# Optimization experiments

Hardware: AMD Instinct MI355X
Metric: run time of the kernel (lower is better)

## Reference

```python
import jax, jax.numpy as jnp
import numpy as np

NUM_CLASSES = 10
HIDDEN = 64
_LABEL2MASK_THRESHOL = 500


def setup_inputs() -> dict:
    key = jax.random.key(0)
    ks = jax.random.split(key, 8)
    B, h, w = 4, 60, 80
    feature1 = jax.random.normal(ks[0], (B, 512, h, w), dtype=jnp.float32)
    feature2 = jax.random.normal(ks[1], (B, 512, h // 2, w // 2), dtype=jnp.float32)
    # kaiming fan_in init for 1x1 convs: std = sqrt(2/fan_in)
    w1 = jax.random.normal(ks[2], (HIDDEN, 512), dtype=jnp.float32) * np.sqrt(2.0 / 512)
    b1 = jnp.zeros((HIDDEN,), dtype=jnp.float32)
    w2 = jax.random.normal(ks[3], (HIDDEN, 512), dtype=jnp.float32) * np.sqrt(2.0 / 512)
    b2 = jnp.zeros((HIDDEN,), dtype=jnp.float32)
    wo = jax.random.normal(ks[4], (NUM_CLASSES + 1, HIDDEN), dtype=jnp.float32) * np.sqrt(2.0 / HIDDEN)
    bo = jnp.zeros((NUM_CLASSES + 1,), dtype=jnp.float32)
    return {"feature1": feature1, "feature2": feature2, "w1": w1, "b1": b1,
            "w2": w2, "b2": b2, "wo": wo, "bo": bo}


def conv1x1(x, w, b):
    # x: (B,C,H,W), w: (O,C) -> (B,O,H,W)
    return jnp.einsum('bchw,oc->bohw', x, w) + b[None, :, None, None]


def label2bbx(seg, num_classes):
    # seg: (B,H,W) int labels. Vectorized per-(batch,class) min/max reduction
    # replacing the original python double loop. Fixed output shape
    # (B*(num_classes-1), 6); rows failing the pixel-count threshold are -1.
    B, H, W = seg.shape
    classes = jnp.arange(1, num_classes)  # cls_id != 0, covers 1..num_classes-1
    mask = seg[:, None, :, :] == classes[None, :, None, None]  # (B,C-1,H,W)
    count = mask.sum(axis=(2, 3))
    xs = jnp.arange(W)
    ys = jnp.arange(H)
    big = jnp.int32(2 ** 30)
    xmin = jnp.where(mask, xs[None, None, None, :], big).min(axis=(2, 3))
    xmax = jnp.where(mask, xs[None, None, None, :], -1).max(axis=(2, 3))
    ymin = jnp.where(mask, ys[None, None, :, None], big).min(axis=(2, 3))
    ymax = jnp.where(mask, ys[None, None, :, None], -1).max(axis=(2, 3))
    valid = count >= _LABEL2MASK_THRESHOL
    batch_ids = jnp.broadcast_to(jnp.arange(B)[:, None], (B, num_classes - 1))
    cls_ids = jnp.broadcast_to(classes[None, :], (B, num_classes - 1))
    rows = jnp.stack([batch_ids, xmin, ymin, xmax, ymax, cls_ids], axis=-1)
    rows = jnp.where(valid[..., None], rows, -1)
    return rows.reshape(-1, 6)


def reference(feature1, feature2, w1, b1, w2, b2, wo, bo):
    feat1 = jax.nn.relu(conv1x1(feature1, w1, b1))          # (B,64,h,w)
    feat2 = jax.nn.relu(conv1x1(feature2, w2, b2))          # (B,64,h/2,w/2)
    feat2_up = jnp.repeat(jnp.repeat(feat2, 2, axis=2), 2, axis=3)
    combo = feat1 + feat2_up
    # nearest upsample scale_factor=8
    combo_up = jnp.repeat(jnp.repeat(combo, 8, axis=2), 8, axis=3)  # (B,64,8h,8w)
    out = jax.nn.relu(conv1x1(combo_up, wo, bo))            # (B,11,8h,8w)
    probability = jax.nn.softmax(out, axis=1)
    segmentation = jnp.argmax(probability, axis=1)
    bbx = label2bbx(segmentation, NUM_CLASSES)
    return probability, segmentation, bbx
```

## Files before the change

### kernel.cpp

```cpp
#include <hip/hip_runtime.h>
#include <math.h>

#define NB   4
#define CIN  512
#define HID  64
#define NK   11
#define HH1  60
#define W1p  80
#define P1   4800
#define HH2  30
#define W2p  40
#define P2   1200
#define HO   480
#define WOp  640
#define NP1  (NB*P1)
#define NP2  (NB*P2)
#define PLANE ((size_t)HO*WOp)
#define SEG_OFF ((size_t)NB*NK*PLANE)
#define BBX_OFF (SEG_OFF + (size_t)NB*PLANE)

#define WS_C1  65536
#define WS_F2  (WS_C1 + NP1*64)
#define WS_PRB (WS_F2 + NP2*64)
#define WS_SEG (WS_PRB + NP1*12)

typedef __attribute__((ext_vector_type(8))) short bf16x8;
typedef __attribute__((ext_vector_type(4))) float f32x4;

__device__ __forceinline__ unsigned short bfsplit(float x, float& resid) {
    unsigned u = __float_as_uint(x);
    unsigned t = u + 0x7FFFu + ((u >> 16) & 1u);
    unsigned short h = (unsigned short)(t >> 16);
    resid = x - __uint_as_float((unsigned)h << 16);
    return h;
}

__device__ __forceinline__ void gld16(const void* g, void* l) {
    __builtin_amdgcn_global_load_lds(
        (const __attribute__((address_space(1))) void*)g,
        (__attribute__((address_space(3))) void*)l, 16, 0, 0);
}

__global__ __launch_bounds__(256) void pack_w(const float* __restrict__ w1,
                                              const float* __restrict__ w2,
                                              float* __restrict__ ws) {
    int i = blockIdx.x * 256 + threadIdx.x;
    if (i >= HID * CIN) return;
    int o = i >> 9, c = i & 511;
    int chunk = c >> 6, r = c & 63, ks2 = r >> 5, k = r & 31;
    int lane = (o & 15) + ((k >> 3) << 4);
    int mt = o >> 4;
    int d = ((((chunk * 2 + ks2) * 4 + mt) * 2) * 64 + lane) * 8 + (k & 7);
    unsigned short* q = (unsigned short*)ws;
    float r1;
    unsigned short h = bfsplit(w1[i], r1);
    unsigned short m = bfsplit(r1, r1);
    q[d] = h; q[d + 512] = m;
    h = bfsplit(w2[i], r1); m = bfsplit(r1, r1);
    q[65536 + d] = h; q[65536 + d + 512] = m;
}

__global__ __launch_bounds__(256) void conv_mfma(const float* __restrict__ f1,
                                                 const float* __restrict__ f2,
                                                 const float* __restrict__ b1v,
                                                 const float* __restrict__ b2v,
                                                 const float* __restrict__ wsbase,
                                                 float* __restrict__ c1o,
                                                 float* __restrict__ f2o) {
    __shared__ float xraw[2][4096];
    __shared__ int   alds[2][4096];
    __shared__ int   xpl[4096];
    int t = blockIdx.x;
    const float* X; const float* bias; float* Cout; const int* WPK;
    int P, px0;
    const unsigned short* q = (const unsigned short*)wsbase;
    if (t < 300) {
        int b = t / 75, ti = t % 75;
        px0 = ti * 64;
        X = f1 + (size_t)b * CIN * P1;  P = P1;  bias = b1v;
        WPK = (const int*)q;
        Cout = c1o + (size_t)b * P1 * 64;
    } else {
        int u = t - 300; int b = u / 19, ti = u % 19;
        px0 = ti * 64; if (px0 > P2 - 64) px0 = P2 - 64;
        X = f2 + (size_t)b * CIN * P2;  P = P2;  bias = b2v;
        WPK = (const int*)(q + 65536);
        Cout = f2o + (size_t)b * P2 * 64;
    }
    int tid  = threadIdx.x;
    int lane = tid & 63;
    int wv   = tid >> 6;
    int pcol = lane & 15, kgrp = lane >> 4;

    auto dmaX = [&](int cc, int buf) {
#pragma unroll
        for (int qq = 0; qq < 4; ++qq) {
            int k = wv * 4 + qq;
            const float* g = X + (size_t)(cc * 64 + k * 4 + (lane >> 4)) * P
                           + px0 + (lane & 15) * 4;
            gld16(g, (void*)&xraw[buf][k * 256]);
        }
    };
    auto dmaA = [&](int cc, int buf) {
#pragma unroll
        for (int qq = 0; qq < 4; ++qq) {
            int k = wv * 4 + qq;
            const int* g = WPK + cc * 4096 + k * 256 + lane * 4;
            gld16(g, (void*)&alds[buf][k * 256]);
        }
    };
    auto convert = [&](int buf) {
        int pxl = wv * 16 + pcol;
#pragma unroll
        for (int ks2 = 0; ks2 < 2; ++ks2) {
            int hh[8], mm[8];
#pragma unroll
            for (int j = 0; j < 8; ++j) {
                float x = xraw[buf][(ks2 * 32 + kgrp * 8 + j) * 64 + pxl];
                float r;
                unsigned short h = bfsplit(x, r);
                unsigned short m = bfsplit(r, r);
                hh[j] = h; mm[j] = m;
            }
            int4 H, M;
            ((int*)&H)[0] = hh[0] | (hh[1] << 16); ((int*)&H)[1] = hh[2] | (hh[3] << 16);
            ((int*)&H)[2] = hh[4] | (hh[5] << 16); ((int*)&H)[3] = hh[6] | (hh[7] << 16);
            ((int*)&M)[0] = mm[0] | (mm[1] << 16); ((int*)&M)[1] = mm[2] | (mm[3] << 16);
            ((int*)&M)[2] = mm[4] | (mm[5] << 16); ((int*)&M)[3] = mm[6] | (mm[7] << 16);
            int pg = ((wv * 2 + ks2) * 2) * 256 + lane * 4;
            *(int4*)&xpl[pg]       = H;
            *(int4*)&xpl[pg + 256] = M;
        }
    };

    union FU { int4 q; bf16x8 v; };
    f32x4 acc[4];
#pragma unroll
    for (int st = 0; st < 4; ++st) acc[st] = (f32x4){0.f, 0.f, 0.f, 0.f};

    dmaX(0, 0); dmaA(0, 0);
    __syncthreads();

    int cur = 0;
    for (int c = 0; c < 8; ++c) {
        if (c < 7) { dmaX(c + 1, cur ^ 1); dmaA(c + 1, cur ^ 1); }
        convert(cur);
        asm volatile("s_waitcnt lgkmcnt(0)" ::: "memory");
        __builtin_amdgcn_s_barrier();
        __builtin_amdgcn_sched_barrier(0);
#pragma unroll
        for (int ks2 = 0; ks2 < 2; ++ks2) {
            FU Ah, Am;
            int pa = ((ks2 * 4 + wv) * 2) * 256 + lane * 4;
            Ah.q = *(const int4*)&alds[cur][pa];
            Am.q = *(const int4*)&alds[cur][pa + 256];
#pragma unroll
            for (int st = 0; st < 4; ++st) {
                FU Bh, Bm;
                int pb = ((st * 2 + ks2) * 2) * 256 + lane * 4;
                Bh.q = *(const int4*)&xpl[pb];
                Bm.q = *(const int4*)&xpl[pb + 256];
                acc[st] = __builtin_amdgcn_mfma_f32_16x16x32_bf16(Ah.v, Bh.v, acc[st], 0, 0, 0);
                acc[st] = __builtin_amdgcn_mfma_f32_16x16x32_bf16(Ah.v, Bm.v, acc[st], 0, 0, 0);
                acc[st] = __builtin_amdgcn_mfma_f32_16x16x32_bf16(Am.v, Bh.v, acc[st], 0, 0, 0);
                acc[st] = __builtin_amdgcn_mfma_f32_16x16x32_bf16(Am.v, Bm.v, acc[st], 0, 0, 0);
            }
        }
        __builtin_amdgcn_sched_barrier(0);
        __syncthreads();
        cur ^= 1;
    }

    int r4 = (lane >> 4) * 4;
    float4 bb = *(const float4*)(bias + wv * 16 + r4);
#pragma unroll
    for (int st = 0; st < 4; ++st) {
        int px = px0 + st * 16 + pcol;
        float a0 = acc[st][0] + bb.x;
        float a1 = acc[st][1] + bb.y;
        float a2 = acc[st][2] + bb.z;
        float a3 = acc[st][3] + bb.w;
        *(float4*)(Cout + (size_t)px * 64 + wv * 16 + r4) =
            make_float4(a0 > 0.f ? a0 : 0.f, a1 > 0.f ? a1 : 0.f,
                        a2 > 0.f ? a2 : 0.f, a3 > 0.f ? a3 : 0.f);
    }
}

__global__ __launch_bounds__(256) void head_kernel(const float* __restrict__ wo,
                                                   const float* __restrict__ bo,
                                                   float* __restrict__ ws) {
    __shared__ float swo[NK * 64];
    __shared__ float sbo[NK];
    for (int i = threadIdx.x; i < NK * 64; i += 256) swo[i] = wo[i];
    if (threadIdx.x < NK) sbo[threadIdx.x] = bo[threadIdx.x];
    __syncthreads();

    int p  = blockIdx.x * 256 + threadIdx.x;
    int b  = p / P1;
    int pb = p % P1;
    int y  = pb / W1p, x = pb % W1p;
    int qp = (y >> 1) * W2p + (x >> 1);
    const float* c1p = ws + WS_C1 + ((size_t)b * P1 + pb) * 64;
    const float* f2p = ws + WS_F2 + ((size_t)b * P2 + qp) * 64;

    float ok[NK];
#pragma unroll
    for (int k = 0; k < NK; ++k) ok[k] = sbo[k];
#pragma unroll
    for (int o4 = 0; o4 < 16; ++o4) {
        float4 c1q = *(const float4*)(c1p + o4 * 4);
        float4 f2q = *(const float4*)(f2p + o4 * 4);
        float co[4] = { c1q.x + f2q.x, c1q.y + f2q.y, c1q.z + f2q.z, c1q.w + f2q.w };
#pragma unroll
        for (int j = 0; j < 4; ++j) {
            int o = o4 * 4 + j;
#pragma unroll
            for (int k = 0; k < NK; ++k) ok[k] = fmaf(co[j], swo[k * 64 + o], ok[k]);
        }
    }
    float m = 0.f;
#pragma unroll
    for (int k = 0; k < NK; ++k) {
        ok[k] = ok[k] > 0.f ? ok[k] : 0.f;
        if (ok[k] > m) m = ok[k];
    }
    float e[NK], sum = 0.f;
#pragma unroll
    for (int k = 0; k < NK; ++k) { e[k] = expf(ok[k] - m); sum += e[k]; }
    float inv = 1.f / sum;
    int arg = 0; float best = ok[0];
#pragma unroll
    for (int k = 1; k < NK; ++k) { if (ok[k] > best) { best = ok[k]; arg = k; } }

    float* pr = ws + WS_PRB + (size_t)p * 12;
#pragma unroll
    for (int k = 0; k < NK; ++k) pr[k] = e[k] * inv;
    pr[11] = (float)arg;
    ((int*)(ws + WS_SEG))[p] = arg;
}

__global__ __launch_bounds__(256) void upsample_kernel(const float* __restrict__ ws,
                                                       float* __restrict__ out) {
    const float* prb = ws + WS_PRB;
    unsigned total4 = (unsigned)((SEG_OFF + (size_t)NB * PLANE) / 4);
    unsigned step = gridDim.x * 256;
    for (unsigned i4 = blockIdx.x * 256 + threadIdx.x; i4 < total4; i4 += step) {
        unsigned f = i4 * 4;
        float v;
        if (f < (unsigned)SEG_OFF) {
            unsigned plane = f / (unsigned)PLANE;
            unsigned r = f - plane * (unsigned)PLANE;
            unsigned b = plane / NK, k = plane - b * NK;
            unsigned y = r / WOp, x = r - y * WOp;
            unsigned p = b * P1 + (y >> 3) * W1p + (x >> 3);
            v = prb[p * 12 + k];
        } else {
            unsigned g = f - (unsigned)SEG_OFF;
            unsigned b = g / (unsigned)PLANE;
            unsigned r = g - b * (unsigned)PLANE;
            unsigned y = r / WOp, x = r - y * WOp;
            unsigned p = b * P1 + (y >> 3) * W1p + (x >> 3);
            v = prb[p * 12 + 11];
        }
        *(float4*)(out + f) = make_float4(v, v, v, v);
    }
}

__global__ __launch_bounds__(256) void bbx_kernel(const float* __restrict__ ws,
                                                  float* __restrict__ out) {
    __shared__ int cnt[10], xmn[10], xmx[10], ymn[10], ymx[10];
    int b = blockIdx.x;
    int t = threadIdx.x;
    if (t < 10) { cnt[t] = 0; xmn[t] = 1 << 30; xmx[t] = -1; ymn[t] = 1 << 30; ymx[t] = -1; }
    __syncthreads();
    const int* seg = (const int*)(ws + WS_SEG) + b * P1;
    for (int p = t; p < P1; p += 256) {
        int s = seg[p];
        if (s >= 1 && s <= 9) {
            int y = p / W1p, x = p % W1p;
            atomicAdd(&cnt[s], 1);
            atomicMin(&xmn[s], x); atomicMax(&xmx[s], x);
            atomicMin(&ymn[s], y); atomicMax(&ymx[s], y);
        }
    }
    __syncthreads();
    if (t < 9) {
        int c = t + 1;
        bool valid = cnt[c] * 64 >= 500;
        float r[6];
        if (valid) {
            r[0] = (float)b;
            r[1] = (float)(xmn[c] * 8);
            r[2] = (float)(ymn[c] * 8);
            r[3] = (float)(xmx[c] * 8 + 7);
            r[4] = (float)(ymx[c] * 8 + 7);
            r[5] = (float)c;
        } else {
            for (int i = 0; i < 6; ++i) r[i] = -1.f;
        }
        float* row = out + BBX_OFF + (size_t)(b * 9 + t) * 6;
        for (int i = 0; i < 6; ++i) row[i] = r[i];
    }
}

extern "C" void kernel_launch(void* const* d_in, const int* in_sizes, int n_in,
                              void* d_out, int out_size, void* d_ws, size_t ws_size,
                              hipStream_t stream) {
    const float* f1 = (const float*)d_in[0];
    const float* f2 = (const float*)d_in[1];
    const float* w1 = (const float*)d_in[2];
    const float* b1 = (const float*)d_in[3];
    const float* w2 = (const float*)d_in[4];
    const float* b2 = (const float*)d_in[5];
    const float* wo = (const float*)d_in[6];
    const float* bo = (const float*)d_in[7];
    float* ws  = (float*)d_ws;
    float* out = (float*)d_out;

    pack_w<<<128, 256, 0, stream>>>(w1, w2, ws);
    conv_mfma<<<376, 256, 0, stream>>>(f1, f2, b1, b2, ws,
                                       ws + WS_C1, ws + WS_F2);
    head_kernel<<<75, 256, 0, stream>>>(wo, bo, ws);
    upsample_kernel<<<2048, 256, 0, stream>>>(ws, out);
    bbx_kernel<<<NB, 256, 0, stream>>>(ws, out);
}
```

Before: 55.73 us.

## Fuse head softmax/argmax with 8x upsample write into one kernel

```diff
diff --git a/kernel.cpp b/kernel.cpp
--- a/kernel.cpp
+++ b/kernel.cpp
@@ -21,8 +21,7 @@
 
 #define WS_C1  65536
 #define WS_F2  (WS_C1 + NP1*64)
-#define WS_PRB (WS_F2 + NP2*64)
-#define WS_SEG (WS_PRB + NP1*12)
+#define WS_SEG (WS_F2 + NP2*64)
 
 typedef __attribute__((ext_vector_type(8))) short bf16x8;
 typedef __attribute__((ext_vector_type(4))) float f32x4;
@@ -186,83 +185,78 @@
     }
 }
 
-__global__ __launch_bounds__(256) void head_kernel(const float* __restrict__ wo,
-                                                   const float* __restrict__ bo,
-                                                   float* __restrict__ ws) {
+__global__ __launch_bounds__(1024) void up_head(const float* __restrict__ wo,
+                                                const float* __restrict__ bo,
+                                                float* __restrict__ ws,
+                                                float* __restrict__ out) {
+    __shared__ float prob[64 * 13];
     __shared__ float swo[NK * 64];
     __shared__ float sbo[NK];
-    for (int i = threadIdx.x; i < NK * 64; i += 256) swo[i] = wo[i];
-    if (threadIdx.x < NK) sbo[threadIdx.x] = bo[threadIdx.x];
-    __syncthreads();
-
-    int p  = blockIdx.x * 256 + threadIdx.x;
-    int b  = p / P1;
-    int pb = p % P1;
-    int y  = pb / W1p, x = pb % W1p;
-    int qp = (y >> 1) * W2p + (x >> 1);
-    const float* c1p = ws + WS_C1 + ((size_t)b * P1 + pb) * 64;
-    const float* f2p = ws + WS_F2 + ((size_t)b * P2 + qp) * 64;
-
-    float ok[NK];
-#pragma unroll
-    for (int k = 0; k < NK; ++k) ok[k] = sbo[k];
-#pragma unroll
-    for (int o4 = 0; o4 < 16; ++o4) {
-        float4 c1q = *(const float4*)(c1p + o4 * 4);
-        float4 f2q = *(const float4*)(f2p + o4 * 4);
-        float co[4] = { c1q.x + f2q.x, c1q.y + f2q.y, c1q.z + f2q.z, c1q.w + f2q.w };
-#pragma unroll
-        for (int j = 0; j < 4; ++j) {
-            int o = o4 * 4 + j;
-#pragma unroll
-            for (int k = 0; k < NK; ++k) ok[k] = fmaf(co[j], swo[k * 64 + o], ok[k]);
-        }
-    }
-    float m = 0.f;
-#pragma unroll
-    for (int k = 0; k < NK; ++k) {
-        ok[k] = ok[k] > 0.f ? ok[k] : 0.f;
-        if (ok[k] > m) m = ok[k];
-    }
-    float e[NK], sum = 0.f;
-#pragma unroll
-    for (int k = 0; k < NK; ++k) { e[k] = expf(ok[k] - m); sum += e[k]; }
-    float inv = 1.f / sum;
-    int arg = 0; float best = ok[0];
-#pragma unroll
-    for (int k = 1; k < NK; ++k) { if (ok[k] > best) { best = ok[k]; arg = k; } }
-
-    float* pr = ws + WS_PRB + (size_t)p * 12;
-#pragma unroll
-    for (int k = 0; k < NK; ++k) pr[k] = e[k] * inv;
-    pr[11] = (float)arg;
-    ((int*)(ws + WS_SEG))[p] = arg;
-}
-
-__global__ __launch_bounds__(256) void upsample_kernel(const float* __restrict__ ws,
-                                                       float* __restrict__ out) {
-    const float* prb = ws + WS_PRB;
-    unsigned total4 = (unsigned)((SEG_OFF + (size_t)NB * PLANE) / 4);
-    unsigned step = gridDim.x * 256;
-    for (unsigned i4 = blockIdx.x * 256 + threadIdx.x; i4 < total4; i4 += step) {
-        unsigned f = i4 * 4;
-        float v;
-        if (f < (unsigned)SEG_OFF) {
-            unsigned plane = f / (unsigned)PLANE;
-            unsigned r = f - plane * (unsigned)PLANE;
-            unsigned b = plane / NK, k = plane - b * NK;
-            unsigned y = r / WOp, x = r - y * WOp;
-            unsigned p = b * P1 + (y >> 3) * W1p + (x >> 3);
-            v = prb[p * 12 + k];
-        } else {
-            unsigned g = f - (unsigned)SEG_OFF;
-            unsigned b = g / (unsigned)PLANE;
-            unsigned r = g - b * (unsigned)PLANE;
-            unsigned y = r / WOp, x = r - y * WOp;
-            unsigned p = b * P1 + (y >> 3) * W1p + (x >> 3);
-            v = prb[p * 12 + 11];
-        }
-        *(float4*)(out + f) = make_float4(v, v, v, v);
+    int t = blockIdx.x;
+    int b = t / 75, ti = t % 75;
+    int px0 = ti * 64;
+    int tid = threadIdx.x;
+    for (int i = tid; i < NK * 64; i += 1024) swo[i] = wo[i];
+    if (tid < NK) sbo[tid] = bo[tid];
+    __syncthreads();
+
+    if (tid < 64) {
+        int px_g = px0 + tid;
+        int y = px_g / W1p, x = px_g % W1p;
+        int qp = (y >> 1) * W2p + (x >> 1);
+        const float* c1p = ws + WS_C1 + ((size_t)b * P1 + px_g) * 64;
+        const float* f2p = ws + WS_F2 + ((size_t)b * P2 + qp) * 64;
+        float ok[NK];
+#pragma unroll
+        for (int k = 0; k < NK; ++k) ok[k] = sbo[k];
+#pragma unroll
+        for (int o4 = 0; o4 < 16; ++o4) {
+            float4 cq = *(const float4*)(c1p + o4 * 4);
+            float4 fq = *(const float4*)(f2p + o4 * 4);
+            float co[4] = { cq.x + fq.x, cq.y + fq.y, cq.z + fq.z, cq.w + fq.w };
+#pragma unroll
+            for (int j = 0; j < 4; ++j) {
+                int o = o4 * 4 + j;
+#pragma unroll
+                for (int k = 0; k < NK; ++k) ok[k] = fmaf(co[j], swo[k * 64 + o], ok[k]);
+            }
+        }
+        float m = 0.f;
+#pragma unroll
+        for (int k = 0; k < NK; ++k) {
+            ok[k] = ok[k] > 0.f ? ok[k] : 0.f;
+            if (ok[k] > m) m = ok[k];
+        }
+        float e[NK], sum = 0.f;
+#pragma unroll
+        for (int k = 0; k < NK; ++k) { e[k] = expf(ok[k] - m); sum += e[k]; }
+        float inv = 1.f / sum;
+        int arg = 0; float best = ok[0];
+#pragma unroll
+        for (int k = 1; k < NK; ++k) { if (ok[k] > best) { best = ok[k]; arg = k; } }
+#pragma unroll
+        for (int k = 0; k < NK; ++k) prob[tid * 13 + k] = e[k] * inv;
+        prob[tid * 13 + 11] = (float)arg;
+        ((int*)(ws + WS_SEG))[b * P1 + px_g] = arg;
+    }
+    __syncthreads();
+
+    for (int id = tid; id < 12 * 8 * 128; id += 1024) {
+        int k   = id >> 10;
+        int rem = id & 1023;
+        int dy  = rem >> 7;
+        int g   = rem & 127;
+        int j   = g >> 1;
+        int qq  = g & 1;
+        int px_g = px0 + j;
+        int y = px_g / W1p, x = px_g % W1p;
+        float v = prob[j * 13 + k];
+        size_t base;
+        if (k < NK)
+            base = (((size_t)(b * NK + k) * HO) + (size_t)(y * 8 + dy)) * WOp + x * 8 + qq * 4;
+        else
+            base = SEG_OFF + (((size_t)b * HO) + (size_t)(y * 8 + dy)) * WOp + x * 8 + qq * 4;
+        *(float4*)(out + base) = make_float4(v, v, v, v);
     }
 }
 
@@ -320,7 +314,6 @@
     pack_w<<<128, 256, 0, stream>>>(w1, w2, ws);
     conv_mfma<<<376, 256, 0, stream>>>(f1, f2, b1, b2, ws,
                                        ws + WS_C1, ws + WS_F2);
-    head_kernel<<<75, 256, 0, stream>>>(wo, bo, ws);
-    upsample_kernel<<<2048, 256, 0, stream>>>(ws, out);
+    up_head<<<300, 1024, 0, stream>>>(wo, bo, ws, out);
     bbx_kernel<<<NB, 256, 0, stream>>>(ws, out);
 }
```

Result: slower. 63.91 us (+14.7%).

## Use triple-buffered 32-channel chunks with explicit vmcnt waits in conv kernel

Applied to the files above, without the earlier changes.

```diff
diff --git a/kernel.cpp b/kernel.cpp
--- a/kernel.cpp
+++ b/kernel.cpp
@@ -67,9 +67,9 @@
                                                  const float* __restrict__ wsbase,
                                                  float* __restrict__ c1o,
                                                  float* __restrict__ f2o) {
-    __shared__ float xraw[2][4096];
-    __shared__ int   alds[2][4096];
-    __shared__ int   xpl[4096];
+    __shared__ float xraw[3][2048];
+    __shared__ int   alds2[2][2048];
+    __shared__ int   xpl[2048];
     int t = blockIdx.x;
     const float* X; const float* bias; float* Cout; const int* WPK;
     int P, px0;
@@ -92,45 +92,46 @@
     int wv   = tid >> 6;
     int pcol = lane & 15, kgrp = lane >> 4;
 
+    int r4 = (lane >> 4) * 4;
+    float4 bb = *(const float4*)(bias + wv * 16 + r4);
+    __builtin_amdgcn_sched_barrier(0);
+
     auto dmaX = [&](int cc, int buf) {
 #pragma unroll
-        for (int qq = 0; qq < 4; ++qq) {
-            int k = wv * 4 + qq;
-            const float* g = X + (size_t)(cc * 64 + k * 4 + (lane >> 4)) * P
+        for (int qq = 0; qq < 2; ++qq) {
+            int k = wv * 2 + qq;
+            const float* g = X + (size_t)(cc * 32 + k * 4 + (lane >> 4)) * P
                            + px0 + (lane & 15) * 4;
             gld16(g, (void*)&xraw[buf][k * 256]);
         }
     };
     auto dmaA = [&](int cc, int buf) {
 #pragma unroll
-        for (int qq = 0; qq < 4; ++qq) {
-            int k = wv * 4 + qq;
-            const int* g = WPK + cc * 4096 + k * 256 + lane * 4;
-            gld16(g, (void*)&alds[buf][k * 256]);
+        for (int qq = 0; qq < 2; ++qq) {
+            int k = wv * 2 + qq;
+            const int* g = WPK + cc * 2048 + k * 256 + lane * 4;
+            gld16(g, (void*)&alds2[buf][k * 256]);
         }
     };
     auto convert = [&](int buf) {
         int pxl = wv * 16 + pcol;
-#pragma unroll
-        for (int ks2 = 0; ks2 < 2; ++ks2) {
-            int hh[8], mm[8];
-#pragma unroll
-            for (int j = 0; j < 8; ++j) {
-                float x = xraw[buf][(ks2 * 32 + kgrp * 8 + j) * 64 + pxl];
-                float r;
-                unsigned short h = bfsplit(x, r);
-                unsigned short m = bfsplit(r, r);
-                hh[j] = h; mm[j] = m;
-            }
-            int4 H, M;
-            ((int*)&H)[0] = hh[0] | (hh[1] << 16); ((int*)&H)[1] = hh[2] | (hh[3] << 16);
-            ((int*)&H)[2] = hh[4] | (hh[5] << 16); ((int*)&H)[3] = hh[6] | (hh[7] << 16);
-            ((int*)&M)[0] = mm[0] | (mm[1] << 16); ((int*)&M)[1] = mm[2] | (mm[3] << 16);
-            ((int*)&M)[2] = mm[4] | (mm[5] << 16); ((int*)&M)[3] = mm[6] | (mm[7] << 16);
-            int pg = ((wv * 2 + ks2) * 2) * 256 + lane * 4;
-            *(int4*)&xpl[pg]       = H;
-            *(int4*)&xpl[pg + 256] = M;
-        }
+        int hh[8], mm[8];
+#pragma unroll
+        for (int j = 0; j < 8; ++j) {
+            float x = xraw[buf][(kgrp * 8 + j) * 64 + pxl];
+            float r;
+            unsigned short h = bfsplit(x, r);
+            unsigned short m = bfsplit(r, r);
+            hh[j] = h; mm[j] = m;
+        }
+        int4 H, M;
+        ((int*)&H)[0] = hh[0] | (hh[1] << 16); ((int*)&H)[1] = hh[2] | (hh[3] << 16);
+        ((int*)&H)[2] = hh[4] | (hh[5] << 16); ((int*)&H)[3] = hh[6] | (hh[7] << 16);
+        ((int*)&M)[0] = mm[0] | (mm[1] << 16); ((int*)&M)[1] = mm[2] | (mm[3] << 16);
+        ((int*)&M)[2] = mm[4] | (mm[5] << 16); ((int*)&M)[3] = mm[6] | (mm[7] << 16);
+        int pg = (wv * 2) * 256 + lane * 4;
+        *(int4*)&xpl[pg]       = H;
+        *(int4*)&xpl[pg + 256] = M;
     };
 
     union FU { int4 q; bf16x8 v; };
@@ -138,26 +139,32 @@
 #pragma unroll
     for (int st = 0; st < 4; ++st) acc[st] = (f32x4){0.f, 0.f, 0.f, 0.f};
 
-    dmaX(0, 0); dmaA(0, 0);
-    __syncthreads();
-
-    int cur = 0;
-    for (int c = 0; c < 8; ++c) {
-        if (c < 7) { dmaX(c + 1, cur ^ 1); dmaA(c + 1, cur ^ 1); }
-        convert(cur);
-        asm volatile("s_waitcnt lgkmcnt(0)" ::: "memory");
+    dmaX(0, 0); dmaX(1, 1); dmaA(0, 0);
+
+    for (int c = 0; c < 16; ++c) {
+        if (c + 2 < 16) dmaX(c + 2, (c + 2) % 3);
+        if (c == 0 || c == 14) asm volatile("s_waitcnt vmcnt(6)" ::: "memory");
+        else if (c == 15)      asm volatile("s_waitcnt vmcnt(4)" ::: "memory");
+        else                   asm volatile("s_waitcnt vmcnt(8)" ::: "memory");
         __builtin_amdgcn_s_barrier();
         __builtin_amdgcn_sched_barrier(0);
-#pragma unroll
-        for (int ks2 = 0; ks2 < 2; ++ks2) {
+        if (c + 1 < 16) dmaA(c + 1, (c + 1) & 1);
+        convert(c % 3);
+        if (c <= 13)      asm volatile("s_waitcnt vmcnt(4) lgkmcnt(0)" ::: "memory");
+        else if (c == 14) asm volatile("s_waitcnt vmcnt(2) lgkmcnt(0)" ::: "memory");
+        else              asm volatile("s_waitcnt vmcnt(0) lgkmcnt(0)" ::: "memory");
+        __builtin_amdgcn_s_barrier();
+        __builtin_amdgcn_sched_barrier(0);
+        {
             FU Ah, Am;
-            int pa = ((ks2 * 4 + wv) * 2) * 256 + lane * 4;
-            Ah.q = *(const int4*)&alds[cur][pa];
-            Am.q = *(const int4*)&alds[cur][pa + 256];
+            int cur2 = c & 1;
+            int pa = (wv * 2) * 256 + lane * 4;
+            Ah.q = *(const int4*)&alds2[cur2][pa];
+            Am.q = *(const int4*)&alds2[cur2][pa + 256];
 #pragma unroll
             for (int st = 0; st < 4; ++st) {
                 FU Bh, Bm;
-                int pb = ((st * 2 + ks2) * 2) * 256 + lane * 4;
+                int pb = (st * 2) * 256 + lane * 4;
                 Bh.q = *(const int4*)&xpl[pb];
                 Bm.q = *(const int4*)&xpl[pb + 256];
                 acc[st] = __builtin_amdgcn_mfma_f32_16x16x32_bf16(Ah.v, Bh.v, acc[st], 0, 0, 0);
@@ -166,13 +173,8 @@
                 acc[st] = __builtin_amdgcn_mfma_f32_16x16x32_bf16(Am.v, Bm.v, acc[st], 0, 0, 0);
             }
         }
-        __builtin_amdgcn_sched_barrier(0);
-        __syncthreads();
-        cur ^= 1;
-    }
-
-    int r4 = (lane >> 4) * 4;
-    float4 bb = *(const float4*)(bias + wv * 16 + r4);
+    }
+
 #pragma unroll
     for (int st = 0; st < 4; ++st) {
         int px = px0 + st * 16 + pcol;
```

New measurement: 57.51 us. 3.2% more time.
